# Optimization experiments

Hardware: AMD Instinct MI355X
Metric: run time of the kernel (lower is better)

Reference implementation:

```python
import jax, jax.numpy as jnp
import numpy as np

DIM = 512
HEADS = 8
DIM_HEAD = 64
INNER = HEADS * DIM_HEAD  # 512
EPS = 1e-5


def _per_head_layernorm(t, gamma, beta):
    # t: [b, h, n, k]; gamma/beta: [h, k] (distinct LayerNorm per head)
    mu = jnp.mean(t, axis=-1, keepdims=True)
    var = jnp.mean(jnp.square(t - mu), axis=-1, keepdims=True)
    t_hat = (t - mu) * jax.lax.rsqrt(var + EPS)
    return t_hat * gamma[None, :, None, :] + beta[None, :, None, :]


def setup_inputs() -> dict:
    key = jax.random.key(0)
    ks = jax.random.split(key, 6)
    x = jax.random.normal(ks[0], (4, 8192, DIM), dtype=jnp.float32)
    # xavier_normal_ with gain=1e-4 on to_qkv weight [3*inner, dim]
    std_qkv = 1e-4 * np.sqrt(2.0 / (3 * INNER + DIM))
    W_qkv = jax.random.normal(ks[1], (3 * INNER, DIM), dtype=jnp.float32) * std_qkv
    gamma_K = jnp.ones((HEADS, DIM_HEAD), dtype=jnp.float32)
    beta_K = jnp.zeros((HEADS, DIM_HEAD), dtype=jnp.float32)
    gamma_V = jnp.ones((HEADS, DIM_HEAD), dtype=jnp.float32)
    beta_V = jnp.zeros((HEADS, DIM_HEAD), dtype=jnp.float32)
    std_out = np.sqrt(1.0 / INNER)
    W_out = jax.random.uniform(ks[2], (DIM, INNER), dtype=jnp.float32, minval=-std_out, maxval=std_out)
    b_out = jax.random.uniform(ks[3], (DIM,), dtype=jnp.float32, minval=-std_out, maxval=std_out)
    return {"x": x, "W_qkv": W_qkv, "gamma_K": gamma_K, "beta_K": beta_K,
            "gamma_V": gamma_V, "beta_V": beta_V, "W_out": W_out, "b_out": b_out}


def reference(x, W_qkv, gamma_K, beta_K, gamma_V, beta_V, W_out, b_out):
    b, n, _ = x.shape
    qkv = jnp.einsum('bnd,ed->bne', x, W_qkv)  # [b, n, 3*inner]
    q, k, v = jnp.split(qkv, 3, axis=-1)

    def to_heads(t):  # [b, n, h*k] -> [b, h, n, k]
        return t.reshape(b, n, HEADS, DIM_HEAD).transpose(0, 2, 1, 3)

    q, k, v = to_heads(q), to_heads(k), to_heads(v)
    k = _per_head_layernorm(k, gamma_K, beta_K)
    v = _per_head_layernorm(v, gamma_V, beta_V)

    # Galerkin linear attention: (K^T V)/n then Q @ (.)  -> O(n * d^2)
    p_attn = jnp.einsum('bhnk,bhnv->bhkv', k, v) / n  # [b, h, k, k]
    out = jnp.einsum('bhnk,bhkv->bhnv', q, p_attn)    # [b, h, n, k]
    out = out.transpose(0, 2, 1, 3).reshape(b, n, INNER)
    return jnp.einsum('bne,de->bnd', out, W_out) + b_out
```

## Files before the change

### kernel.cpp

```cpp
#include <hip/hip_runtime.h>


typedef __attribute__((ext_vector_type(8))) short bf16x8;
typedef __attribute__((ext_vector_type(4))) float f32x4;
typedef __attribute__((ext_vector_type(4))) unsigned short u16x4;

__device__ __forceinline__ unsigned short f2bf(float f) {
  unsigned int u = __builtin_bit_cast(unsigned int, f);
  u += 0x7FFFu + ((u >> 16) & 1u);
  return (unsigned short)(u >> 16);
}

__device__ __forceinline__ f32x4 mfma16(bf16x8 a, bf16x8 b, f32x4 c) {
  return __builtin_amdgcn_mfma_f32_16x16x32_bf16(a, b, c, 0, 0, 0);
}

__device__ __forceinline__ void gload16(const void* g, void* l) {
  __builtin_amdgcn_global_load_lds(
      (const __attribute__((address_space(1))) void*)g,
      (__attribute__((address_space(3))) void*)l, 16, 0, 0);
}

__global__ void k_cvt_bf16(const float* __restrict__ src,
                           unsigned short* __restrict__ dst, int n4) {
  int i = blockIdx.x * blockDim.x + threadIdx.x;
  if (i < n4) {
    float4 v = ((const float4*)src)[i];
    u16x4 o;
    o[0] = f2bf(v.x); o[1] = f2bf(v.y); o[2] = f2bf(v.z); o[3] = f2bf(v.w);
    ((u16x4*)dst)[i] = o;
  }
}

__device__ __forceinline__ void stage_tile(const unsigned short* pa,
                                           const unsigned short* pb,
                                           unsigned short* As, unsigned short* Bs,
                                           int w) {
#pragma unroll
  for (int j = 0; j < 4; ++j) {
    gload16(pa + j * 8 * 512, As + w * 2048 + j * 512);
    gload16(pb + j * 8 * 512, Bs + w * 2048 + j * 512);
  }
}

__device__ __forceinline__ void compute_tile(const unsigned short* As,
                                             const unsigned short* Bs,
                                             int wr, int wc, int g, int c16,
                                             f32x4 acc[4][4]) {
#pragma unroll
  for (int ks = 0; ks < 2; ++ks) {
    const int kcol = (ks * 32 + g * 8) ^ ((c16 & 7) << 3);
    bf16x8 af[4], bfv[4];
#pragma unroll
    for (int mi = 0; mi < 4; ++mi)
      af[mi] = *(const bf16x8*)&As[(wr * 64 + mi * 16 + c16) * 64 + kcol];
#pragma unroll
    for (int ni = 0; ni < 4; ++ni)
      bfv[ni] = *(const bf16x8*)&Bs[(wc * 64 + ni * 16 + c16) * 64 + kcol];
#pragma unroll
    for (int mi = 0; mi < 4; ++mi)
#pragma unroll
      for (int ni = 0; ni < 4; ++ni)
        acc[mi][ni] = mfma16(af[mi], bfv[ni], acc[mi][ni]);
  }
}

__launch_bounds__(256)
__global__ void k1_kvp(const unsigned short* __restrict__ xb,
                       const unsigned short* __restrict__ wqkvb,
                       const float* __restrict__ gK, const float* __restrict__ bK,
                       const float* __restrict__ gV, const float* __restrict__ bV,
                       float* __restrict__ Ppart) {
  __shared__ __align__(16) unsigned short As[8192];
  __shared__ __align__(16) unsigned short Bs[8192];
  const int bid = (int)blockIdx.x;
  const int wgid = (bid & 7) * 256 + (bid >> 3);
  const int rt = wgid >> 3, h = wgid & 7;
  const int tid = (int)threadIdx.x;
  const int l = tid & 63, w = tid >> 6;
  const int wr = w >> 1, wc = w & 1;
  const int g = l >> 4, c16 = l & 15;
  const int row0 = rt * 128;
  const int swz = ((l & 7) ^ (l >> 3)) * 8;

  const unsigned short* gsA = xb + (row0 + w * 32 + (l >> 3)) * 512 + swz;
  const int bcol = (w < 2) ? (512 + h * 64 + w * 32) : (1024 + h * 64 + (w - 2) * 32);
  const unsigned short* gsB = wqkvb + (bcol + (l >> 3)) * 512 + swz;

  f32x4 acc[4][4] = {};
  for (int kt = 0; kt < 8; ++kt) {
    stage_tile(gsA + kt * 64, gsB + kt * 64, As, Bs, w);
    __syncthreads();
    compute_tile(As, Bs, wr, wc, g, c16, acc);
    __syncthreads();
  }

  const float* gamma = (wc == 0) ? gK : gV;
  const float* beta  = (wc == 0) ? bK : bV;
  float gm[4], bt[4];
#pragma unroll
  for (int ni = 0; ni < 4; ++ni) {
    gm[ni] = gamma[h * 64 + ni * 16 + c16];
    bt[ni] = beta[h * 64 + ni * 16 + c16];
  }

  unsigned short* dst = (wc == 0) ? As : Bs;
#pragma unroll
  for (int mi = 0; mi < 4; ++mi) {
    float mean4[4], rs4[4];
#pragma unroll
    for (int r = 0; r < 4; ++r) {
      float a0 = acc[mi][0][r], a1 = acc[mi][1][r];
      float a2 = acc[mi][2][r], a3 = acc[mi][3][r];
      float s1 = a0 + a1 + a2 + a3;
      float s2 = a0 * a0 + a1 * a1 + a2 * a2 + a3 * a3;
#pragma unroll
      for (int m = 1; m <= 8; m <<= 1) {
        s1 += __shfl_xor(s1, m, 64);
        s2 += __shfl_xor(s2, m, 64);
      }
      const float mean = s1 * (1.0f / 64.0f);
      const float var = s2 * (1.0f / 64.0f) - mean * mean;
      mean4[r] = mean;
      rs4[r] = rsqrtf(var + 1e-5f);
    }
    const int n0 = wr * 64 + mi * 16 + g * 4;
#pragma unroll
    for (int ni = 0; ni < 4; ++ni) {
      u16x4 o;
#pragma unroll
      for (int r = 0; r < 4; ++r)
        o[r] = f2bf((acc[mi][ni][r] - mean4[r]) * rs4[r] * gm[ni] + bt[ni]);
      *(u16x4*)&dst[(ni * 16 + c16) * 128 + (((n0 >> 3) ^ c16) << 3) + (n0 & 7)] = o;
    }
  }
  __syncthreads();

  f32x4 pacc[4] = {};
#pragma unroll
  for (int ks = 0; ks < 4; ++ks) {
    const int grp = ((ks * 4 + g) ^ c16) << 3;
    bf16x8 af = *(const bf16x8*)&As[(w * 16 + c16) * 128 + grp];
#pragma unroll
    for (int ni = 0; ni < 4; ++ni) {
      bf16x8 bv = *(const bf16x8*)&Bs[(ni * 16 + c16) * 128 + grp];
      pacc[ni] = mfma16(af, bv, pacc[ni]);
    }
  }
  const int bh = (rt >> 6) * 8 + h;
  float* Pp = Ppart + ((size_t)(bh * 64 + (rt & 63))) * 4096;
#pragma unroll
  for (int ni = 0; ni < 4; ++ni)
#pragma unroll
    for (int r = 0; r < 4; ++r)
      Pp[(w * 16 + g * 4 + r) * 64 + ni * 16 + c16] = pacc[ni][r];
}

__launch_bounds__(256)
__global__ void k_preduce(const float* __restrict__ Ppart,
                          float* __restrict__ P) {
  const int bh = blockIdx.x;
  const int e = blockIdx.y * 256 + threadIdx.x;
  const float* src = Ppart + (size_t)bh * 64 * 4096 + e;
  float s = 0.f;
#pragma unroll 8
  for (int sl = 0; sl < 64; ++sl) s += src[sl * 4096];
  P[bh * 4096 + e] = s;
}

__launch_bounds__(256)
__global__ void k3a_g(const float* __restrict__ Wqkv,
                      const float* __restrict__ P,
                      unsigned short* __restrict__ Gt) {
  __shared__ float Pl[64 * 64];
  const int bh = blockIdx.x, dd = blockIdx.y;
  const int b = bh >> 3, h = bh & 7;
  const int t = (int)threadIdx.x;
  for (int i = t; i < 1024; i += 256)
    ((float4*)Pl)[i] = ((const float4*)(P + bh * 4096))[i];
  __syncthreads();

  const int qg = t >> 6, dl = t & 63;
  const int d = dd * 64 + dl;
  float acc[16] = {};
  for (int dh = 0; dh < 64; ++dh) {
    const float wq = Wqkv[(h * 64 + dh) * 512 + d];
    const float* pr = &Pl[dh * 64 + qg * 16];
#pragma unroll
    for (int i = 0; i < 16; ++i) acc[i] += pr[i] * wq;
  }
  unsigned short* go = &Gt[(b * 512 + d) * 512 + h * 64 + qg * 16];
#pragma unroll
  for (int i = 0; i < 16; ++i) go[i] = f2bf(acc[i] * (1.0f / 8192.0f));
}

__launch_bounds__(256)
__global__ void k3b_m(const unsigned short* __restrict__ wob,
                      const unsigned short* __restrict__ Gt,
                      unsigned short* __restrict__ Mb) {
  __shared__ __align__(16) unsigned short As[8192];
  __shared__ __align__(16) unsigned short Bs[8192];
  const int rt = blockIdx.x, ct = blockIdx.y, b = blockIdx.z;
  const int tid = (int)threadIdx.x;
  const int l = tid & 63, w = tid >> 6;
  const int wr = w >> 1, wc = w & 1;
  const int g = l >> 4, c16 = l & 15;
  const int row0 = rt * 128, col0 = ct * 128;
  const int swz = ((l & 7) ^ (l >> 3)) * 8;

  const unsigned short* gsA = wob + (row0 + w * 32 + (l >> 3)) * 512 + swz;
  const unsigned short* gsB = Gt + b * 262144 + (col0 + w * 32 + (l >> 3)) * 512 + swz;

  f32x4 acc[4][4] = {};
  for (int kt = 0; kt < 8; ++kt) {
    stage_tile(gsA + kt * 64, gsB + kt * 64, As, Bs, w);
    __syncthreads();
    compute_tile(As, Bs, wr, wc, g, c16, acc);
    __syncthreads();
  }

#pragma unroll
  for (int mi = 0; mi < 4; ++mi)
#pragma unroll
    for (int ni = 0; ni < 4; ++ni) {
      const int colg = col0 + wc * 64 + ni * 16 + c16;
#pragma unroll
      for (int r = 0; r < 4; ++r) {
        const int rowg = row0 + wr * 64 + mi * 16 + g * 4 + r;
        Mb[(b * 512 + rowg) * 512 + colg] = f2bf(acc[mi][ni][r]);
      }
    }
}

__launch_bounds__(256)
__global__ void k4_final(const unsigned short* __restrict__ xb,
                         const unsigned short* __restrict__ Mb,
                         const float* __restrict__ bout,
                         float* __restrict__ y) {
  __shared__ __align__(16) unsigned short As[8192];
  __shared__ __align__(16) unsigned short Bs[8192];
  const int bid = (int)blockIdx.x;
  const int wgid = (bid & 7) * 128 + (bid >> 3);
  const int rt = wgid >> 2, ct = wgid & 3;
  const int tid = (int)threadIdx.x;
  const int l = tid & 63, w = tid >> 6;
  const int wr = w >> 1, wc = w & 1;
  const int g = l >> 4, c16 = l & 15;
  const int row0 = rt * 128, col0 = ct * 128;
  const int bb = row0 >> 13;
  const int swz = ((l & 7) ^ (l >> 3)) * 8;

  const unsigned short* gsA = xb + (row0 + w * 32 + (l >> 3)) * 512 + swz;
  const unsigned short* gsB = Mb + bb * 262144 + (col0 + w * 32 + (l >> 3)) * 512 + swz;

  f32x4 acc[4][4] = {};
  for (int kt = 0; kt < 8; ++kt) {
    stage_tile(gsA + kt * 64, gsB + kt * 64, As, Bs, w);
    __syncthreads();
    compute_tile(As, Bs, wr, wc, g, c16, acc);
    __syncthreads();
  }

  float bo[4];
#pragma unroll
  for (int ni = 0; ni < 4; ++ni)
    bo[ni] = bout[col0 + wc * 64 + ni * 16 + c16];
#pragma unroll
  for (int mi = 0; mi < 4; ++mi)
#pragma unroll
    for (int ni = 0; ni < 4; ++ni) {
      const int colg = col0 + wc * 64 + ni * 16 + c16;
#pragma unroll
      for (int r = 0; r < 4; ++r) {
        const int rowg = row0 + wr * 64 + mi * 16 + g * 4 + r;
        y[rowg * 512 + colg] = acc[mi][ni][r] + bo[ni];
      }
    }
}

extern "C" void kernel_launch(void* const* d_in, const int* in_sizes, int n_in,
                              void* d_out, int out_size, void* d_ws, size_t ws_size,
                              hipStream_t stream) {
  (void)in_sizes; (void)n_in; (void)out_size; (void)ws_size;
  const float* x    = (const float*)d_in[0];
  const float* Wqkv = (const float*)d_in[1];
  const float* gK   = (const float*)d_in[2];
  const float* bK   = (const float*)d_in[3];
  const float* gV   = (const float*)d_in[4];
  const float* bV   = (const float*)d_in[5];
  const float* Wout = (const float*)d_in[6];
  const float* bout = (const float*)d_in[7];
  float* y = (float*)d_out;

  char* w = (char*)d_ws;
  unsigned short* xb    = (unsigned short*)(w);
  unsigned short* Wb    = (unsigned short*)(w + 33554432);
  unsigned short* Wob   = (unsigned short*)(w + 35127296);
  float*          P     = (float*)         (w + 35651584);
  unsigned short* Gt    = (unsigned short*)(w + 36175872);
  unsigned short* Mb    = (unsigned short*)(w + 38273024);
  float*          Ppart = (float*)         (w + 40370176);

  k_cvt_bf16<<<16384, 256, 0, stream>>>(x, xb, 4194304);
  k_cvt_bf16<<<768, 256, 0, stream>>>(Wqkv, Wb, 196608);
  k_cvt_bf16<<<256, 256, 0, stream>>>(Wout, Wob, 65536);

  k1_kvp<<<2048, 256, 0, stream>>>(xb, Wb, gK, bK, gV, bV, Ppart);
  k_preduce<<<dim3(32, 16), 256, 0, stream>>>(Ppart, P);
  k3a_g<<<dim3(32, 8), 256, 0, stream>>>(Wqkv, P, Gt);
  k3b_m<<<dim3(4, 4, 4), 256, 0, stream>>>(Wob, Gt, Mb);
  k4_final<<<1024, 256, 0, stream>>>(xb, Mb, bout, y);
}
```

Baseline: 133.6 us.

## Process two heads per workgroup in K/V projection to reuse staged x tile

Each k1_kvp workgroup now computes K/V projections for two heads (h and h+4), sharing one staged x tile across both heads' weight tiles. This halves the grid size and the redundant global/LDS loads of the x row tile. The cost is doubled accumulator registers (two 4x4 f32x4 sets), more LDS, and a launch bound of 2 waves per SIMD. The layernorm and P-partial epilogue then run sequentially for each head.

```diff
diff --git a/kernel.cpp b/kernel.cpp
--- a/kernel.cpp
+++ b/kernel.cpp
@@ -65,17 +65,19 @@
   }
 }
 
-__launch_bounds__(256)
+__launch_bounds__(256, 2)
 __global__ void k1_kvp(const unsigned short* __restrict__ xb,
                        const unsigned short* __restrict__ wqkvb,
                        const float* __restrict__ gK, const float* __restrict__ bK,
                        const float* __restrict__ gV, const float* __restrict__ bV,
                        float* __restrict__ Ppart) {
   __shared__ __align__(16) unsigned short As[8192];
-  __shared__ __align__(16) unsigned short Bs[8192];
+  __shared__ __align__(16) unsigned short Bs0[8192];
+  __shared__ __align__(16) unsigned short Bs1[8192];
   const int bid = (int)blockIdx.x;
-  const int wgid = (bid & 7) * 256 + (bid >> 3);
-  const int rt = wgid >> 3, h = wgid & 7;
+  const int wgid = (bid & 7) * 128 + (bid >> 3);
+  const int rt = wgid >> 2, hp = wgid & 3;
+  const int h0 = hp, h1 = hp + 4;
   const int tid = (int)threadIdx.x;
   const int l = tid & 63, w = tid >> 6;
   const int wr = w >> 1, wc = w & 1;
@@ -84,76 +86,113 @@
   const int swz = ((l & 7) ^ (l >> 3)) * 8;
 
   const unsigned short* gsA = xb + (row0 + w * 32 + (l >> 3)) * 512 + swz;
-  const int bcol = (w < 2) ? (512 + h * 64 + w * 32) : (1024 + h * 64 + (w - 2) * 32);
-  const unsigned short* gsB = wqkvb + (bcol + (l >> 3)) * 512 + swz;
-
-  f32x4 acc[4][4] = {};
+  const int bc0 = (w < 2) ? (512 + h0 * 64 + w * 32) : (1024 + h0 * 64 + (w - 2) * 32);
+  const int bc1 = (w < 2) ? (512 + h1 * 64 + w * 32) : (1024 + h1 * 64 + (w - 2) * 32);
+  const unsigned short* gsB0 = wqkvb + (bc0 + (l >> 3)) * 512 + swz;
+  const unsigned short* gsB1 = wqkvb + (bc1 + (l >> 3)) * 512 + swz;
+
+  f32x4 acc0[4][4] = {};
+  f32x4 acc1[4][4] = {};
   for (int kt = 0; kt < 8; ++kt) {
-    stage_tile(gsA + kt * 64, gsB + kt * 64, As, Bs, w);
-    __syncthreads();
-    compute_tile(As, Bs, wr, wc, g, c16, acc);
-    __syncthreads();
-  }
-
-  const float* gamma = (wc == 0) ? gK : gV;
-  const float* beta  = (wc == 0) ? bK : bV;
-  float gm[4], bt[4];
-#pragma unroll
-  for (int ni = 0; ni < 4; ++ni) {
-    gm[ni] = gamma[h * 64 + ni * 16 + c16];
-    bt[ni] = beta[h * 64 + ni * 16 + c16];
-  }
-
-  unsigned short* dst = (wc == 0) ? As : Bs;
-#pragma unroll
-  for (int mi = 0; mi < 4; ++mi) {
-    float mean4[4], rs4[4];
-#pragma unroll
-    for (int r = 0; r < 4; ++r) {
-      float a0 = acc[mi][0][r], a1 = acc[mi][1][r];
-      float a2 = acc[mi][2][r], a3 = acc[mi][3][r];
-      float s1 = a0 + a1 + a2 + a3;
-      float s2 = a0 * a0 + a1 * a1 + a2 * a2 + a3 * a3;
-#pragma unroll
-      for (int m = 1; m <= 8; m <<= 1) {
-        s1 += __shfl_xor(s1, m, 64);
-        s2 += __shfl_xor(s2, m, 64);
-      }
-      const float mean = s1 * (1.0f / 64.0f);
-      const float var = s2 * (1.0f / 64.0f) - mean * mean;
-      mean4[r] = mean;
-      rs4[r] = rsqrtf(var + 1e-5f);
-    }
-    const int n0 = wr * 64 + mi * 16 + g * 4;
+    const unsigned short* pa = gsA + kt * 64;
+    const unsigned short* pb0 = gsB0 + kt * 64;
+    const unsigned short* pb1 = gsB1 + kt * 64;
+#pragma unroll
+    for (int j = 0; j < 4; ++j) {
+      gload16(pa + j * 8 * 512, As + w * 2048 + j * 512);
+      gload16(pb0 + j * 8 * 512, Bs0 + w * 2048 + j * 512);
+      gload16(pb1 + j * 8 * 512, Bs1 + w * 2048 + j * 512);
+    }
+    __syncthreads();
+#pragma unroll
+    for (int ks = 0; ks < 2; ++ks) {
+      const int kcol = (ks * 32 + g * 8) ^ ((c16 & 7) << 3);
+      bf16x8 af[4], bf0[4], bf1[4];
+#pragma unroll
+      for (int mi = 0; mi < 4; ++mi)
+        af[mi] = *(const bf16x8*)&As[(wr * 64 + mi * 16 + c16) * 64 + kcol];
+#pragma unroll
+      for (int ni = 0; ni < 4; ++ni) {
+        bf0[ni] = *(const bf16x8*)&Bs0[(wc * 64 + ni * 16 + c16) * 64 + kcol];
+        bf1[ni] = *(const bf16x8*)&Bs1[(wc * 64 + ni * 16 + c16) * 64 + kcol];
+      }
+#pragma unroll
+      for (int mi = 0; mi < 4; ++mi)
+#pragma unroll
+        for (int ni = 0; ni < 4; ++ni) {
+          acc0[mi][ni] = mfma16(af[mi], bf0[ni], acc0[mi][ni]);
+          acc1[mi][ni] = mfma16(af[mi], bf1[ni], acc1[mi][ni]);
+        }
+    }
+    __syncthreads();
+  }
+
+  const int bb = rt >> 6;
+  const int slab = rt & 63;
+#pragma unroll
+  for (int hidx = 0; hidx < 2; ++hidx) {
+    const int h = hidx ? h1 : h0;
+    f32x4 (*acc)[4] = hidx ? acc1 : acc0;
+    const float* gamma = (wc == 0) ? gK : gV;
+    const float* beta  = (wc == 0) ? bK : bV;
+    float gm[4], bt[4];
 #pragma unroll
     for (int ni = 0; ni < 4; ++ni) {
-      u16x4 o;
+      gm[ni] = gamma[h * 64 + ni * 16 + c16];
+      bt[ni] = beta[h * 64 + ni * 16 + c16];
+    }
+    unsigned short* dst = (wc == 0) ? As : Bs0;
+#pragma unroll
+    for (int mi = 0; mi < 4; ++mi) {
+      float mean4[4], rs4[4];
+#pragma unroll
+      for (int r = 0; r < 4; ++r) {
+        float a0 = acc[mi][0][r], a1 = acc[mi][1][r];
+        float a2 = acc[mi][2][r], a3 = acc[mi][3][r];
+        float s1 = a0 + a1 + a2 + a3;
+        float s2 = a0 * a0 + a1 * a1 + a2 * a2 + a3 * a3;
+#pragma unroll
+        for (int m = 1; m <= 8; m <<= 1) {
+          s1 += __shfl_xor(s1, m, 64);
+          s2 += __shfl_xor(s2, m, 64);
+        }
+        const float mean = s1 * (1.0f / 64.0f);
+        const float var = s2 * (1.0f / 64.0f) - mean * mean;
+        mean4[r] = mean;
+        rs4[r] = rsqrtf(var + 1e-5f);
+      }
+      const int n0 = wr * 64 + mi * 16 + g * 4;
+#pragma unroll
+      for (int ni = 0; ni < 4; ++ni) {
+        u16x4 o;
+#pragma unroll
+        for (int r = 0; r < 4; ++r)
+          o[r] = f2bf((acc[mi][ni][r] - mean4[r]) * rs4[r] * gm[ni] + bt[ni]);
+        *(u16x4*)&dst[(ni * 16 + c16) * 128 + (((n0 >> 3) ^ c16) << 3) + (n0 & 7)] = o;
+      }
+    }
+    __syncthreads();
+
+    f32x4 pacc[4] = {};
+#pragma unroll
+    for (int ks = 0; ks < 4; ++ks) {
+      const int grp = ((ks * 4 + g) ^ c16) << 3;
+      bf16x8 af = *(const bf16x8*)&As[(w * 16 + c16) * 128 + grp];
+#pragma unroll
+      for (int ni = 0; ni < 4; ++ni) {
+        bf16x8 bv = *(const bf16x8*)&Bs0[(ni * 16 + c16) * 128 + grp];
+        pacc[ni] = mfma16(af, bv, pacc[ni]);
+      }
+    }
+    const int bh = bb * 8 + h;
+    float* Pp = Ppart + ((size_t)(bh * 64 + slab)) * 4096;
+#pragma unroll
+    for (int ni = 0; ni < 4; ++ni)
 #pragma unroll
       for (int r = 0; r < 4; ++r)
-        o[r] = f2bf((acc[mi][ni][r] - mean4[r]) * rs4[r] * gm[ni] + bt[ni]);
-      *(u16x4*)&dst[(ni * 16 + c16) * 128 + (((n0 >> 3) ^ c16) << 3) + (n0 & 7)] = o;
-    }
-  }
-  __syncthreads();
-
-  f32x4 pacc[4] = {};
-#pragma unroll
-  for (int ks = 0; ks < 4; ++ks) {
-    const int grp = ((ks * 4 + g) ^ c16) << 3;
-    bf16x8 af = *(const bf16x8*)&As[(w * 16 + c16) * 128 + grp];
-#pragma unroll
-    for (int ni = 0; ni < 4; ++ni) {
-      bf16x8 bv = *(const bf16x8*)&Bs[(ni * 16 + c16) * 128 + grp];
-      pacc[ni] = mfma16(af, bv, pacc[ni]);
-    }
-  }
-  const int bh = (rt >> 6) * 8 + h;
-  float* Pp = Ppart + ((size_t)(bh * 64 + (rt & 63))) * 4096;
-#pragma unroll
-  for (int ni = 0; ni < 4; ++ni)
-#pragma unroll
-    for (int r = 0; r < 4; ++r)
-      Pp[(w * 16 + g * 4 + r) * 64 + ni * 16 + c16] = pacc[ni][r];
+        Pp[(w * 16 + g * 4 + r) * 64 + ni * 16 + c16] = pacc[ni][r];
+    __syncthreads();
+  }
 }
 
 __launch_bounds__(256)
@@ -305,7 +344,7 @@
   k_cvt_bf16<<<768, 256, 0, stream>>>(Wqkv, Wb, 196608);
   k_cvt_bf16<<<256, 256, 0, stream>>>(Wout, Wob, 65536);
 
-  k1_kvp<<<2048, 256, 0, stream>>>(xb, Wb, gK, bK, gV, bV, Ppart);
+  k1_kvp<<<1024, 256, 0, stream>>>(xb, Wb, gK, bK, gV, bV, Ppart);
   k_preduce<<<dim3(32, 16), 256, 0, stream>>>(Ppart, P);
   k3a_g<<<dim3(32, 8), 256, 0, stream>>>(Wqkv, P, Gt);
   k3b_m<<<dim3(4, 4, 4), 256, 0, stream>>>(Wob, Gt, Mb);
```

New measurement: 128.7 us. 3.7% less time.

## Double-buffer A tiles and load B fragments directly from global in k1 and k4

Applied to the files above, without the earlier changes.

In the QKV-projection/LayerNorm kernel and the final output GEMM, the shared B tile is replaced by per-lane direct global loads of the weight fragments into registers. The freed LDS is used to double-buffer the A (x) tile, so the next k-tile is prefetched while the current one is computed, and one of the two barriers per iteration is removed. Launch bounds are raised to request four blocks per CU. The trade-off is redundant global/L2 traffic for B, since each wave now fetches its own fragments, plus higher register pressure from holding bfv[4][2].

```diff
diff --git a/kernel.cpp b/kernel.cpp
--- a/kernel.cpp
+++ b/kernel.cpp
@@ -32,47 +32,13 @@
   }
 }
 
-__device__ __forceinline__ void stage_tile(const unsigned short* pa,
-                                           const unsigned short* pb,
-                                           unsigned short* As, unsigned short* Bs,
-                                           int w) {
-#pragma unroll
-  for (int j = 0; j < 4; ++j) {
-    gload16(pa + j * 8 * 512, As + w * 2048 + j * 512);
-    gload16(pb + j * 8 * 512, Bs + w * 2048 + j * 512);
-  }
-}
-
-__device__ __forceinline__ void compute_tile(const unsigned short* As,
-                                             const unsigned short* Bs,
-                                             int wr, int wc, int g, int c16,
-                                             f32x4 acc[4][4]) {
-#pragma unroll
-  for (int ks = 0; ks < 2; ++ks) {
-    const int kcol = (ks * 32 + g * 8) ^ ((c16 & 7) << 3);
-    bf16x8 af[4], bfv[4];
-#pragma unroll
-    for (int mi = 0; mi < 4; ++mi)
-      af[mi] = *(const bf16x8*)&As[(wr * 64 + mi * 16 + c16) * 64 + kcol];
-#pragma unroll
-    for (int ni = 0; ni < 4; ++ni)
-      bfv[ni] = *(const bf16x8*)&Bs[(wc * 64 + ni * 16 + c16) * 64 + kcol];
-#pragma unroll
-    for (int mi = 0; mi < 4; ++mi)
-#pragma unroll
-      for (int ni = 0; ni < 4; ++ni)
-        acc[mi][ni] = mfma16(af[mi], bfv[ni], acc[mi][ni]);
-  }
-}
-
-__launch_bounds__(256)
+__launch_bounds__(256, 4)
 __global__ void k1_kvp(const unsigned short* __restrict__ xb,
                        const unsigned short* __restrict__ wqkvb,
                        const float* __restrict__ gK, const float* __restrict__ bK,
                        const float* __restrict__ gV, const float* __restrict__ bV,
                        float* __restrict__ Ppart) {
-  __shared__ __align__(16) unsigned short As[8192];
-  __shared__ __align__(16) unsigned short Bs[8192];
+  __shared__ __align__(16) unsigned short As[2][8192];
   const int bid = (int)blockIdx.x;
   const int wgid = (bid & 7) * 256 + (bid >> 3);
   const int rt = wgid >> 3, h = wgid & 7;
@@ -84,14 +50,41 @@
   const int swz = ((l & 7) ^ (l >> 3)) * 8;
 
   const unsigned short* gsA = xb + (row0 + w * 32 + (l >> 3)) * 512 + swz;
-  const int bcol = (w < 2) ? (512 + h * 64 + w * 32) : (1024 + h * 64 + (w - 2) * 32);
-  const unsigned short* gsB = wqkvb + (bcol + (l >> 3)) * 512 + swz;
+  const unsigned short* gB =
+      wqkvb + (((wc == 0) ? 512 : 1024) + h * 64 + c16) * 512 + g * 8;
 
   f32x4 acc[4][4] = {};
+
+#pragma unroll
+  for (int j = 0; j < 4; ++j)
+    gload16(gsA + j * 8 * 512, (unsigned short*)As[0] + w * 2048 + j * 512);
+  __syncthreads();
+
   for (int kt = 0; kt < 8; ++kt) {
-    stage_tile(gsA + kt * 64, gsB + kt * 64, As, Bs, w);
-    __syncthreads();
-    compute_tile(As, Bs, wr, wc, g, c16, acc);
+    if (kt < 7) {
+#pragma unroll
+      for (int j = 0; j < 4; ++j)
+        gload16(gsA + (kt + 1) * 64 + j * 8 * 512,
+                (unsigned short*)As[(kt + 1) & 1] + w * 2048 + j * 512);
+    }
+    bf16x8 bfv[4][2];
+#pragma unroll
+    for (int ni = 0; ni < 4; ++ni)
+#pragma unroll
+      for (int ks = 0; ks < 2; ++ks)
+        bfv[ni][ks] = *(const bf16x8*)&gB[ni * 8192 + kt * 64 + ks * 32];
+    const unsigned short* Ab = (const unsigned short*)As[kt & 1];
+#pragma unroll
+    for (int ks = 0; ks < 2; ++ks) {
+      const int kcol = (ks * 32 + g * 8) ^ ((c16 & 7) << 3);
+#pragma unroll
+      for (int mi = 0; mi < 4; ++mi) {
+        bf16x8 af = *(const bf16x8*)&Ab[(wr * 64 + mi * 16 + c16) * 64 + kcol];
+#pragma unroll
+        for (int ni = 0; ni < 4; ++ni)
+          acc[mi][ni] = mfma16(af, bfv[ni][ks], acc[mi][ni]);
+      }
+    }
     __syncthreads();
   }
 
@@ -104,7 +97,7 @@
     bt[ni] = beta[h * 64 + ni * 16 + c16];
   }
 
-  unsigned short* dst = (wc == 0) ? As : Bs;
+  unsigned short* dst = (wc == 0) ? (unsigned short*)As[0] : (unsigned short*)As[1];
 #pragma unroll
   for (int mi = 0; mi < 4; ++mi) {
     float mean4[4], rs4[4];
@@ -136,14 +129,16 @@
   }
   __syncthreads();
 
+  const unsigned short* Kl = (const unsigned short*)As[0];
+  const unsigned short* Vl = (const unsigned short*)As[1];
   f32x4 pacc[4] = {};
 #pragma unroll
   for (int ks = 0; ks < 4; ++ks) {
     const int grp = ((ks * 4 + g) ^ c16) << 3;
-    bf16x8 af = *(const bf16x8*)&As[(w * 16 + c16) * 128 + grp];
+    bf16x8 af = *(const bf16x8*)&Kl[(w * 16 + c16) * 128 + grp];
 #pragma unroll
     for (int ni = 0; ni < 4; ++ni) {
-      bf16x8 bv = *(const bf16x8*)&Bs[(ni * 16 + c16) * 128 + grp];
+      bf16x8 bv = *(const bf16x8*)&Vl[(ni * 16 + c16) * 128 + grp];
       pacc[ni] = mfma16(af, bv, pacc[ni]);
     }
   }
@@ -192,6 +187,39 @@
   unsigned short* go = &Gt[(b * 512 + d) * 512 + h * 64 + qg * 16];
 #pragma unroll
   for (int i = 0; i < 16; ++i) go[i] = f2bf(acc[i] * (1.0f / 8192.0f));
+}
+
+__device__ __forceinline__ void stage_tile(const unsigned short* pa,
+                                           const unsigned short* pb,
+                                           unsigned short* As, unsigned short* Bs,
+                                           int w) {
+#pragma unroll
+  for (int j = 0; j < 4; ++j) {
+    gload16(pa + j * 8 * 512, As + w * 2048 + j * 512);
+    gload16(pb + j * 8 * 512, Bs + w * 2048 + j * 512);
+  }
+}
+
+__device__ __forceinline__ void compute_tile(const unsigned short* As,
+                                             const unsigned short* Bs,
+                                             int wr, int wc, int g, int c16,
+                                             f32x4 acc[4][4]) {
+#pragma unroll
+  for (int ks = 0; ks < 2; ++ks) {
+    const int kcol = (ks * 32 + g * 8) ^ ((c16 & 7) << 3);
+    bf16x8 af[4], bfv[4];
+#pragma unroll
+    for (int mi = 0; mi < 4; ++mi)
+      af[mi] = *(const bf16x8*)&As[(wr * 64 + mi * 16 + c16) * 64 + kcol];
+#pragma unroll
+    for (int ni = 0; ni < 4; ++ni)
+      bfv[ni] = *(const bf16x8*)&Bs[(wc * 64 + ni * 16 + c16) * 64 + kcol];
+#pragma unroll
+    for (int mi = 0; mi < 4; ++mi)
+#pragma unroll
+      for (int ni = 0; ni < 4; ++ni)
+        acc[mi][ni] = mfma16(af[mi], bfv[ni], acc[mi][ni]);
+  }
 }
 
 __launch_bounds__(256)
@@ -232,13 +260,12 @@
     }
 }
 
-__launch_bounds__(256)
+__launch_bounds__(256, 4)
 __global__ void k4_final(const unsigned short* __restrict__ xb,
                          const unsigned short* __restrict__ Mb,
                          const float* __restrict__ bout,
                          float* __restrict__ y) {
-  __shared__ __align__(16) unsigned short As[8192];
-  __shared__ __align__(16) unsigned short Bs[8192];
+  __shared__ __align__(16) unsigned short As[2][8192];
   const int bid = (int)blockIdx.x;
   const int wgid = (bid & 7) * 128 + (bid >> 3);
   const int rt = wgid >> 2, ct = wgid & 3;
@@ -251,13 +278,41 @@
   const int swz = ((l & 7) ^ (l >> 3)) * 8;
 
   const unsigned short* gsA = xb + (row0 + w * 32 + (l >> 3)) * 512 + swz;
-  const unsigned short* gsB = Mb + bb * 262144 + (col0 + w * 32 + (l >> 3)) * 512 + swz;
+  const unsigned short* gB =
+      Mb + (size_t)bb * 262144 + (col0 + wc * 64 + c16) * 512 + g * 8;
 
   f32x4 acc[4][4] = {};
+
+#pragma unroll
+  for (int j = 0; j < 4; ++j)
+    gload16(gsA + j * 8 * 512, (unsigned short*)As[0] + w * 2048 + j * 512);
+  __syncthreads();
+
   for (int kt = 0; kt < 8; ++kt) {
-    stage_tile(gsA + kt * 64, gsB + kt * 64, As, Bs, w);
-    __syncthreads();
-    compute_tile(As, Bs, wr, wc, g, c16, acc);
+    if (kt < 7) {
+#pragma unroll
+      for (int j = 0; j < 4; ++j)
+        gload16(gsA + (kt + 1) * 64 + j * 8 * 512,
+                (unsigned short*)As[(kt + 1) & 1] + w * 2048 + j * 512);
+    }
+    bf16x8 bfv[4][2];
+#pragma unroll
+    for (int ni = 0; ni < 4; ++ni)
+#pragma unroll
+      for (int ks = 0; ks < 2; ++ks)
+        bfv[ni][ks] = *(const bf16x8*)&gB[ni * 8192 + kt * 64 + ks * 32];
+    const unsigned short* Ab = (const unsigned short*)As[kt & 1];
+#pragma unroll
+    for (int ks = 0; ks < 2; ++ks) {
+      const int kcol = (ks * 32 + g * 8) ^ ((c16 & 7) << 3);
+#pragma unroll
+      for (int mi = 0; mi < 4; ++mi) {
+        bf16x8 af = *(const bf16x8*)&Ab[(wr * 64 + mi * 16 + c16) * 64 + kcol];
+#pragma unroll
+        for (int ni = 0; ni < 4; ++ni)
+          acc[mi][ni] = mfma16(af, bfv[ni][ks], acc[mi][ni]);
+      }
+    }
     __syncthreads();
   }
 
```

After: 169.9 us. 27.2% more time.

## Fuse fp32-to-bf16 conversion of x into GEMM kernels with register prefetch

Applied to the files above, without the earlier changes.

Removes the standalone x conversion pass and the bf16 copy of x. k1_kvp and k4_final now read fp32 x directly, convert it in registers, and write it to LDS, while prefetching the next K tile with manual waitcnt and barriers. The two weight conversions are merged into one launch. This saves a full 64MB read plus 32MB write round trip, but x is now read in fp32 twice (by k1 and k4), and the extra registers plus launch_bounds occupancy hints may limit occupancy.

```diff
diff --git a/kernel.cpp b/kernel.cpp
--- a/kernel.cpp
+++ b/kernel.cpp
@@ -4,6 +4,7 @@
 typedef __attribute__((ext_vector_type(8))) short bf16x8;
 typedef __attribute__((ext_vector_type(4))) float f32x4;
 typedef __attribute__((ext_vector_type(4))) unsigned short u16x4;
+typedef __attribute__((ext_vector_type(4))) unsigned int u32x4;
 
 __device__ __forceinline__ unsigned short f2bf(float f) {
   unsigned int u = __builtin_bit_cast(unsigned int, f);
@@ -11,6 +12,10 @@
   return (unsigned short)(u >> 16);
 }
 
+__device__ __forceinline__ unsigned int cvt2(float lo, float hi) {
+  return ((unsigned int)f2bf(hi) << 16) | (unsigned int)f2bf(lo);
+}
+
 __device__ __forceinline__ f32x4 mfma16(bf16x8 a, bf16x8 b, f32x4 c) {
   return __builtin_amdgcn_mfma_f32_16x16x32_bf16(a, b, c, 0, 0, 0);
 }
@@ -21,52 +26,23 @@
       (__attribute__((address_space(3))) void*)l, 16, 0, 0);
 }
 
-__global__ void k_cvt_bf16(const float* __restrict__ src,
-                           unsigned short* __restrict__ dst, int n4) {
-  int i = blockIdx.x * blockDim.x + threadIdx.x;
-  if (i < n4) {
-    float4 v = ((const float4*)src)[i];
-    u16x4 o;
-    o[0] = f2bf(v.x); o[1] = f2bf(v.y); o[2] = f2bf(v.z); o[3] = f2bf(v.w);
-    ((u16x4*)dst)[i] = o;
-  }
-}
-
-__device__ __forceinline__ void stage_tile(const unsigned short* pa,
-                                           const unsigned short* pb,
-                                           unsigned short* As, unsigned short* Bs,
-                                           int w) {
-#pragma unroll
-  for (int j = 0; j < 4; ++j) {
-    gload16(pa + j * 8 * 512, As + w * 2048 + j * 512);
-    gload16(pb + j * 8 * 512, Bs + w * 2048 + j * 512);
-  }
-}
-
-__device__ __forceinline__ void compute_tile(const unsigned short* As,
-                                             const unsigned short* Bs,
-                                             int wr, int wc, int g, int c16,
-                                             f32x4 acc[4][4]) {
-#pragma unroll
-  for (int ks = 0; ks < 2; ++ks) {
-    const int kcol = (ks * 32 + g * 8) ^ ((c16 & 7) << 3);
-    bf16x8 af[4], bfv[4];
-#pragma unroll
-    for (int mi = 0; mi < 4; ++mi)
-      af[mi] = *(const bf16x8*)&As[(wr * 64 + mi * 16 + c16) * 64 + kcol];
-#pragma unroll
-    for (int ni = 0; ni < 4; ++ni)
-      bfv[ni] = *(const bf16x8*)&Bs[(wc * 64 + ni * 16 + c16) * 64 + kcol];
-#pragma unroll
-    for (int mi = 0; mi < 4; ++mi)
-#pragma unroll
-      for (int ni = 0; ni < 4; ++ni)
-        acc[mi][ni] = mfma16(af[mi], bfv[ni], acc[mi][ni]);
-  }
-}
-
-__launch_bounds__(256)
-__global__ void k1_kvp(const unsigned short* __restrict__ xb,
+__global__ void k_cvt_w(const float* __restrict__ Wqkv,
+                        const float* __restrict__ Wout,
+                        unsigned short* __restrict__ Wb,
+                        unsigned short* __restrict__ Wob) {
+  int i = blockIdx.x * 256 + threadIdx.x;
+  const float4* src;
+  u16x4* dst;
+  if (i < 196608) { src = (const float4*)Wqkv + i; dst = (u16x4*)Wb + i; }
+  else { i -= 196608; src = (const float4*)Wout + i; dst = (u16x4*)Wob + i; }
+  float4 v = *src;
+  u16x4 o;
+  o[0] = f2bf(v.x); o[1] = f2bf(v.y); o[2] = f2bf(v.z); o[3] = f2bf(v.w);
+  *dst = o;
+}
+
+__launch_bounds__(256, 3)
+__global__ void k1_kvp(const float* __restrict__ x,
                        const unsigned short* __restrict__ wqkvb,
                        const float* __restrict__ gK, const float* __restrict__ bK,
                        const float* __restrict__ gV, const float* __restrict__ bV,
@@ -83,16 +59,64 @@
   const int row0 = rt * 128;
   const int swz = ((l & 7) ^ (l >> 3)) * 8;
 
-  const unsigned short* gsA = xb + (row0 + w * 32 + (l >> 3)) * 512 + swz;
+  const float* gx = x + (size_t)(row0 + w * 32 + (l >> 3)) * 512 + swz;
   const int bcol = (w < 2) ? (512 + h * 64 + w * 32) : (1024 + h * 64 + (w - 2) * 32);
   const unsigned short* gsB = wqkvb + (bcol + (l >> 3)) * 512 + swz;
+  unsigned short* la = As + w * 2048 + l * 8;
 
   f32x4 acc[4][4] = {};
+  float4 pf[8];
+
+#pragma unroll
+  for (int j = 0; j < 4; ++j) {
+    pf[2 * j]     = *(const float4*)(gx + j * 4096);
+    pf[2 * j + 1] = *(const float4*)(gx + j * 4096 + 4);
+  }
+
   for (int kt = 0; kt < 8; ++kt) {
-    stage_tile(gsA + kt * 64, gsB + kt * 64, As, Bs, w);
-    __syncthreads();
-    compute_tile(As, Bs, wr, wc, g, c16, acc);
-    __syncthreads();
+#pragma unroll
+    for (int j = 0; j < 4; ++j) {
+      u32x4 c;
+      c[0] = cvt2(pf[2 * j].x, pf[2 * j].y);
+      c[1] = cvt2(pf[2 * j].z, pf[2 * j].w);
+      c[2] = cvt2(pf[2 * j + 1].x, pf[2 * j + 1].y);
+      c[3] = cvt2(pf[2 * j + 1].z, pf[2 * j + 1].w);
+      *(u32x4*)(la + j * 512) = c;
+    }
+#pragma unroll
+    for (int j = 0; j < 4; ++j)
+      gload16(gsB + kt * 64 + j * 8 * 512, Bs + w * 2048 + j * 512);
+    __builtin_amdgcn_sched_barrier(0);
+    if (kt < 7) {
+#pragma unroll
+      for (int j = 0; j < 4; ++j) {
+        pf[2 * j]     = *(const float4*)(gx + (kt + 1) * 64 + j * 4096);
+        pf[2 * j + 1] = *(const float4*)(gx + (kt + 1) * 64 + j * 4096 + 4);
+      }
+      asm volatile("s_waitcnt vmcnt(8) lgkmcnt(0)" ::: "memory");
+    } else {
+      asm volatile("s_waitcnt vmcnt(0) lgkmcnt(0)" ::: "memory");
+    }
+    __builtin_amdgcn_sched_barrier(0);
+    __builtin_amdgcn_s_barrier();
+#pragma unroll
+    for (int ks = 0; ks < 2; ++ks) {
+      const int kcol = (ks * 32 + g * 8) ^ ((c16 & 7) << 3);
+      bf16x8 af[4], bfv[4];
+#pragma unroll
+      for (int mi = 0; mi < 4; ++mi)
+        af[mi] = *(const bf16x8*)&As[(wr * 64 + mi * 16 + c16) * 64 + kcol];
+#pragma unroll
+      for (int ni = 0; ni < 4; ++ni)
+        bfv[ni] = *(const bf16x8*)&Bs[(wc * 64 + ni * 16 + c16) * 64 + kcol];
+#pragma unroll
+      for (int mi = 0; mi < 4; ++mi)
+#pragma unroll
+        for (int ni = 0; ni < 4; ++ni)
+          acc[mi][ni] = mfma16(af[mi], bfv[ni], acc[mi][ni]);
+    }
+    __builtin_amdgcn_sched_barrier(0);
+    __builtin_amdgcn_s_barrier();
   }
 
   const float* gamma = (wc == 0) ? gK : gV;
@@ -103,7 +127,6 @@
     gm[ni] = gamma[h * 64 + ni * 16 + c16];
     bt[ni] = beta[h * 64 + ni * 16 + c16];
   }
-
   unsigned short* dst = (wc == 0) ? As : Bs;
 #pragma unroll
   for (int mi = 0; mi < 4; ++mi) {
@@ -192,6 +215,39 @@
   unsigned short* go = &Gt[(b * 512 + d) * 512 + h * 64 + qg * 16];
 #pragma unroll
   for (int i = 0; i < 16; ++i) go[i] = f2bf(acc[i] * (1.0f / 8192.0f));
+}
+
+__device__ __forceinline__ void stage_tile(const unsigned short* pa,
+                                           const unsigned short* pb,
+                                           unsigned short* As, unsigned short* Bs,
+                                           int w) {
+#pragma unroll
+  for (int j = 0; j < 4; ++j) {
+    gload16(pa + j * 8 * 512, As + w * 2048 + j * 512);
+    gload16(pb + j * 8 * 512, Bs + w * 2048 + j * 512);
+  }
+}
+
+__device__ __forceinline__ void compute_tile(const unsigned short* As,
+                                             const unsigned short* Bs,
+                                             int wr, int wc, int g, int c16,
+                                             f32x4 acc[4][4]) {
+#pragma unroll
+  for (int ks = 0; ks < 2; ++ks) {
+    const int kcol = (ks * 32 + g * 8) ^ ((c16 & 7) << 3);
+    bf16x8 af[4], bfv[4];
+#pragma unroll
+    for (int mi = 0; mi < 4; ++mi)
+      af[mi] = *(const bf16x8*)&As[(wr * 64 + mi * 16 + c16) * 64 + kcol];
+#pragma unroll
+    for (int ni = 0; ni < 4; ++ni)
+      bfv[ni] = *(const bf16x8*)&Bs[(wc * 64 + ni * 16 + c16) * 64 + kcol];
+#pragma unroll
+    for (int mi = 0; mi < 4; ++mi)
+#pragma unroll
+      for (int ni = 0; ni < 4; ++ni)
+        acc[mi][ni] = mfma16(af[mi], bfv[ni], acc[mi][ni]);
+  }
 }
 
 __launch_bounds__(256)
@@ -232,8 +288,8 @@
     }
 }
 
-__launch_bounds__(256)
-__global__ void k4_final(const unsigned short* __restrict__ xb,
+__launch_bounds__(256, 3)
+__global__ void k4_final(const float* __restrict__ x,
                          const unsigned short* __restrict__ Mb,
                          const float* __restrict__ bout,
                          float* __restrict__ y) {
@@ -250,15 +306,63 @@
   const int bb = row0 >> 13;
   const int swz = ((l & 7) ^ (l >> 3)) * 8;
 
-  const unsigned short* gsA = xb + (row0 + w * 32 + (l >> 3)) * 512 + swz;
-  const unsigned short* gsB = Mb + bb * 262144 + (col0 + w * 32 + (l >> 3)) * 512 + swz;
+  const float* gx = x + (size_t)(row0 + w * 32 + (l >> 3)) * 512 + swz;
+  const unsigned short* gsB =
+      Mb + (size_t)bb * 262144 + (col0 + w * 32 + (l >> 3)) * 512 + swz;
+  unsigned short* la = As + w * 2048 + l * 8;
 
   f32x4 acc[4][4] = {};
+  float4 pf[8];
+#pragma unroll
+  for (int j = 0; j < 4; ++j) {
+    pf[2 * j]     = *(const float4*)(gx + j * 4096);
+    pf[2 * j + 1] = *(const float4*)(gx + j * 4096 + 4);
+  }
+
   for (int kt = 0; kt < 8; ++kt) {
-    stage_tile(gsA + kt * 64, gsB + kt * 64, As, Bs, w);
-    __syncthreads();
-    compute_tile(As, Bs, wr, wc, g, c16, acc);
-    __syncthreads();
+#pragma unroll
+    for (int j = 0; j < 4; ++j) {
+      u32x4 c;
+      c[0] = cvt2(pf[2 * j].x, pf[2 * j].y);
+      c[1] = cvt2(pf[2 * j].z, pf[2 * j].w);
+      c[2] = cvt2(pf[2 * j + 1].x, pf[2 * j + 1].y);
+      c[3] = cvt2(pf[2 * j + 1].z, pf[2 * j + 1].w);
+      *(u32x4*)(la + j * 512) = c;
+    }
+#pragma unroll
+    for (int j = 0; j < 4; ++j)
+      gload16(gsB + kt * 64 + j * 8 * 512, Bs + w * 2048 + j * 512);
+    __builtin_amdgcn_sched_barrier(0);
+    if (kt < 7) {
+#pragma unroll
+      for (int j = 0; j < 4; ++j) {
+        pf[2 * j]     = *(const float4*)(gx + (kt + 1) * 64 + j * 4096);
+        pf[2 * j + 1] = *(const float4*)(gx + (kt + 1) * 64 + j * 4096 + 4);
+      }
+      asm volatile("s_waitcnt vmcnt(8) lgkmcnt(0)" ::: "memory");
+    } else {
+      asm volatile("s_waitcnt vmcnt(0) lgkmcnt(0)" ::: "memory");
+    }
+    __builtin_amdgcn_sched_barrier(0);
+    __builtin_amdgcn_s_barrier();
+#pragma unroll
+    for (int ks = 0; ks < 2; ++ks) {
+      const int kcol = (ks * 32 + g * 8) ^ ((c16 & 7) << 3);
+      bf16x8 af[4], bfv[4];
+#pragma unroll
+      for (int mi = 0; mi < 4; ++mi)
+        af[mi] = *(const bf16x8*)&As[(wr * 64 + mi * 16 + c16) * 64 + kcol];
+#pragma unroll
+      for (int ni = 0; ni < 4; ++ni)
+        bfv[ni] = *(const bf16x8*)&Bs[(wc * 64 + ni * 16 + c16) * 64 + kcol];
+#pragma unroll
+      for (int mi = 0; mi < 4; ++mi)
+#pragma unroll
+        for (int ni = 0; ni < 4; ++ni)
+          acc[mi][ni] = mfma16(af[mi], bfv[ni], acc[mi][ni]);
+    }
+    __builtin_amdgcn_sched_barrier(0);
+    __builtin_amdgcn_s_barrier();
   }
 
   float bo[4];
@@ -293,21 +397,18 @@
   float* y = (float*)d_out;
 
   char* w = (char*)d_ws;
-  unsigned short* xb    = (unsigned short*)(w);
-  unsigned short* Wb    = (unsigned short*)(w + 33554432);
-  unsigned short* Wob   = (unsigned short*)(w + 35127296);
-  float*          P     = (float*)         (w + 35651584);
-  unsigned short* Gt    = (unsigned short*)(w + 36175872);
-  unsigned short* Mb    = (unsigned short*)(w + 38273024);
-  float*          Ppart = (float*)         (w + 40370176);
-
-  k_cvt_bf16<<<16384, 256, 0, stream>>>(x, xb, 4194304);
-  k_cvt_bf16<<<768, 256, 0, stream>>>(Wqkv, Wb, 196608);
-  k_cvt_bf16<<<256, 256, 0, stream>>>(Wout, Wob, 65536);
-
-  k1_kvp<<<2048, 256, 0, stream>>>(xb, Wb, gK, bK, gV, bV, Ppart);
+  unsigned short* Wb    = (unsigned short*)(w);
+  unsigned short* Wob   = (unsigned short*)(w + 1572864);
+  float*          P     = (float*)         (w + 2097152);
+  unsigned short* Gt    = (unsigned short*)(w + 2621440);
+  unsigned short* Mb    = (unsigned short*)(w + 4718592);
+  float*          Ppart = (float*)         (w + 6815744);
+
+  k_cvt_w<<<1024, 256, 0, stream>>>(Wqkv, Wout, Wb, Wob);
+
+  k1_kvp<<<2048, 256, 0, stream>>>(x, Wb, gK, bK, gV, bV, Ppart);
   k_preduce<<<dim3(32, 16), 256, 0, stream>>>(Ppart, P);
   k3a_g<<<dim3(32, 8), 256, 0, stream>>>(Wqkv, P, Gt);
   k3b_m<<<dim3(4, 4, 4), 256, 0, stream>>>(Wob, Gt, Mb);
-  k4_final<<<1024, 256, 0, stream>>>(xb, Mb, bout, y);
-}
+  k4_final<<<1024, 256, 0, stream>>>(x, Mb, bout, y);
+}
```

New measurement: 127.3 us. -4.7%, faster.
